# Performance work log

Measured on AMD Instinct MI355X. Metric: run time of the kernel, lower is better.

## Reference

```python
import jax, jax.numpy as jnp
import numpy as np
from math import sqrt

B, N, M, HID, NH = 16, 512, 1024, 512, 8
HS = HID // NH  # 64


def layer_norm(x, g, b, eps=1e-5):
    mu = jnp.mean(x, axis=-1, keepdims=True)
    var = jnp.var(x, axis=-1, keepdims=True)
    return (x - mu) * jax.lax.rsqrt(var + eps) * g + b


def apply_moverz(x, s, c):
    # x: [B, L, NH, HS]; s, c: [B, L, 1, HS//2]
    x0, x1 = x[..., 0::2], x[..., 1::2]
    return jnp.concatenate([x0 * c - x1 * s, x1 * c + x0 * s], axis=-1)


def attention(q, k, v, mask):
    # q: [B,Nq,NH,HS], k/v: [B,Nk,NH,HS], mask broadcastable to [B,NH,Nq,Nk]
    attn = jnp.einsum('bnhd,bmhd->bhnm', q, k) / sqrt(HS)
    attn = jnp.where(mask, -jnp.inf, attn)
    attn = jax.nn.softmax(attn, axis=-1)
    x = jnp.einsum('bhnm,bmhd->bnhd', attn, v)
    return x.reshape(x.shape[0], x.shape[1], HID)


def setup_inputs() -> dict:
    key = jax.random.key(0)
    ks = jax.random.split(key, 24)
    inp = {}
    inp['tgt'] = jax.random.normal(ks[0], (B, N, HID), dtype=jnp.float32)
    inp['mem'] = jax.random.normal(ks[1], (B, M, HID), dtype=jnp.float32)
    th_p = jax.random.uniform(ks[2], (B, N, 1, HS // 2), dtype=jnp.float32) * (2 * np.pi)
    th_k = jax.random.uniform(ks[3], (B, M, 1, HS // 2), dtype=jnp.float32) * (2 * np.pi)
    inp['pep_mass_sin'] = jnp.sin(th_p)
    inp['pep_mass_cos'] = jnp.cos(th_p)
    inp['peaks_moverz_sin'] = jnp.sin(th_k)
    inp['peaks_moverz_cos'] = jnp.cos(th_k)
    # causal self-attn mask (True = masked)
    inp['tgt_mask'] = jnp.triu(jnp.ones((N, N), dtype=bool), k=1)[None, None]
    # pad last 64 memory positions
    pad = jnp.arange(M) >= (M - 64)
    inp['mem_key_padding_mask'] = jnp.broadcast_to(pad[None, None, None, :], (B, 1, 1, M))
    s = 0.02
    w = lambda i, shape: jax.random.normal(ks[i], shape, dtype=jnp.float32) * s
    # MaskedMultiHeadAttn params
    inp['mmha_w'] = w(4, (3 * HID, HID)); inp['mmha_b'] = jnp.zeros((3 * HID,), jnp.float32)
    inp['mmha_ow'] = w(5, (HID, HID)); inp['mmha_ob'] = jnp.zeros((HID,), jnp.float32)
    inp['mmha_g'] = jnp.ones((HID,), jnp.float32); inp['mmha_beta'] = jnp.zeros((HID,), jnp.float32)
    # MultiHeadAttn (cross) params
    inp['mha_qw'] = w(6, (HID, HID)); inp['mha_qb'] = jnp.zeros((HID,), jnp.float32)
    inp['mha_kvw'] = w(7, (2 * HID, HID)); inp['mha_kvb'] = jnp.zeros((2 * HID,), jnp.float32)
    inp['mha_ow'] = w(8, (HID, HID)); inp['mha_ob'] = jnp.zeros((HID,), jnp.float32)
    inp['mha_g'] = jnp.ones((HID,), jnp.float32); inp['mha_beta'] = jnp.zeros((HID,), jnp.float32)
    # FFN params (no bias)
    inp['ffn_w1'] = w(9, (4 * HID, HID))
    inp['ffn_w2'] = w(10, (HID, 4 * HID))
    inp['ffn_g'] = jnp.ones((HID,), jnp.float32); inp['ffn_beta'] = jnp.zeros((HID,), jnp.float32)
    return inp


def reference(tgt, mem, pep_mass_sin, pep_mass_cos, peaks_moverz_sin, peaks_moverz_cos,
              tgt_mask, mem_key_padding_mask,
              mmha_w, mmha_b, mmha_ow, mmha_ob, mmha_g, mmha_beta,
              mha_qw, mha_qb, mha_kvw, mha_kvb, mha_ow, mha_ob, mha_g, mha_beta,
              ffn_w1, ffn_w2, ffn_g, ffn_beta):
    # --- masked self-attention ---
    qkv = (tgt @ mmha_w.T + mmha_b).reshape(B, N, NH, 3 * HS)
    q, k, v = jnp.split(qkv, 3, axis=-1)
    x = attention(q, k, v, tgt_mask)
    tgt = layer_norm(x @ mmha_ow.T + mmha_ob + tgt, mmha_g, mmha_beta)
    # --- cross-attention with moverz distance bias ---
    q = (tgt @ mha_qw.T + mha_qb).reshape(B, N, NH, HS)
    q = apply_moverz(q, pep_mass_sin, pep_mass_cos)
    kv = (mem @ mha_kvw.T + mha_kvb).reshape(B, M, NH, 2 * HS)
    k, v = jnp.split(kv, 2, axis=-1)
    k = apply_moverz(k, peaks_moverz_sin, peaks_moverz_cos)
    x = attention(q, k, v, mem_key_padding_mask)
    tgt = layer_norm(x @ mha_ow.T + mha_ob + tgt, mha_g, mha_beta)
    # --- FFN ---
    h = jax.nn.relu(tgt @ ffn_w1.T) @ ffn_w2.T
    tgt = layer_norm(tgt + h, ffn_g, ffn_beta)
    return tgt
```

## Files before the change

### kernel.cpp

```cpp
#include <hip/hip_runtime.h>
#include <hip/hip_bf16.h>

#define BB 16
#define NN 512
#define MM 1024
#define HIDD 512
#define NHH 8

typedef unsigned short ushort_t;
typedef __attribute__((ext_vector_type(8))) short short8;
typedef __attribute__((ext_vector_type(8))) _Float16 half8;
typedef __attribute__((ext_vector_type(4))) _Float16 half4;
typedef __attribute__((ext_vector_type(4))) float f32x4;

__device__ __forceinline__ ushort_t f2bf(float x) {
    unsigned u = __float_as_uint(x);
    u += 0x7fff + ((u >> 16) & 1);
    return (ushort_t)(u >> 16);
}

#define GLD16(g, l) __builtin_amdgcn_global_load_lds(                      \
    (const __attribute__((address_space(1))) void*)(g),                    \
    (__attribute__((address_space(3))) void*)(l), 16, 0, 0)

__device__ __forceinline__ void xcd_swizzle(int& colb, int& rowb) {
    int id = blockIdx.x + blockIdx.y * gridDim.x;
    int C = gridDim.x;
    int xcd = id & 7;
    int slot = id >> 3;
    int rows_per = gridDim.y >> 3;
    colb = slot % C;
    rowb = xcd * rows_per + slot / C;
}

__global__ __launch_bounds__(256)
void gemm_bf(const ushort_t* __restrict__ A, const ushort_t* __restrict__ W,
             const float* __restrict__ bias, float* __restrict__ C,
             ushort_t* __restrict__ Cb, _Float16* __restrict__ Ch,
             int K, int Cout, int relu) {
    __shared__ __align__(16) ushort_t smem[2][8192];
    const int tid = threadIdx.x;
    const int lane = tid & 63;
    const int wid = tid >> 6;
    const int wm = wid >> 1, wn = wid & 1;
    int colb, rowb;
    xcd_swizzle(colb, rowb);
    const long row0 = (long)rowb * 128;
    const long col0 = (long)colb * 128;

    const int sr = lane >> 2;
    const int skq = lane & 3;
    const ushort_t* Ag = A + (row0 + wid * 32 + sr) * (long)K + skq * 8;
    const ushort_t* Wg = W + (col0 + wid * 32 + sr) * (long)K + skq * 8;
    const int sa0 = (wid * 32) * 32, sa1 = (wid * 32 + 16) * 32;

    f32x4 acc[4][4] = {};
    const int lr = lane & 15;
    const int kg = lane >> 4;

    GLD16(Ag, &smem[0][sa0]);
    GLD16(Ag + 16 * (long)K, &smem[0][sa1]);
    GLD16(Wg, &smem[0][4096 + sa0]);
    GLD16(Wg + 16 * (long)K, &smem[0][4096 + sa1]);

    int pb = 0;
    for (int k0 = 0; k0 < K; k0 += 32, pb ^= 1) {
        __syncthreads();
        int kn = k0 + 32;
        if (kn < K) {
            GLD16(Ag + kn, &smem[pb ^ 1][sa0]);
            GLD16(Ag + 16 * (long)K + kn, &smem[pb ^ 1][sa1]);
            GLD16(Wg + kn, &smem[pb ^ 1][4096 + sa0]);
            GLD16(Wg + 16 * (long)K + kn, &smem[pb ^ 1][4096 + sa1]);
        }
        const ushort_t* Ab = smem[pb];
        const ushort_t* Wb = smem[pb] + 4096;
        short8 af[4], bfr[4];
#pragma unroll
        for (int i = 0; i < 4; i++)
            af[i] = *(const short8*)&Ab[(wm * 64 + i * 16 + lr) * 32 + kg * 8];
#pragma unroll
        for (int j = 0; j < 4; j++)
            bfr[j] = *(const short8*)&Wb[(wn * 64 + j * 16 + lr) * 32 + kg * 8];
#pragma unroll
        for (int i = 0; i < 4; i++)
#pragma unroll
            for (int j = 0; j < 4; j++)
                acc[i][j] = __builtin_amdgcn_mfma_f32_16x16x32_bf16(
                    af[i], bfr[j], acc[i][j], 0, 0, 0);
    }

#pragma unroll
    for (int i = 0; i < 4; i++) {
#pragma unroll
        for (int j = 0; j < 4; j++) {
            long row = row0 + wm * 64 + i * 16 + kg * 4;
            long col = col0 + wn * 64 + j * 16 + lr;
            float bv = bias ? bias[col] : 0.f;
#pragma unroll
            for (int r = 0; r < 4; r++) {
                float x = acc[i][j][r] + bv;
                if (relu) x = fmaxf(x, 0.f);
                size_t idx = (row + r) * (size_t)Cout + col;
                if (Ch)      Ch[idx] = (_Float16)x;
                else if (Cb) Cb[idx] = f2bf(x);
                else         C[idx] = x;
            }
        }
    }
}

__global__ __launch_bounds__(256)
void gemm_bf64(const ushort_t* __restrict__ A, const ushort_t* __restrict__ W,
               const float* __restrict__ bias, float* __restrict__ C,
               ushort_t* __restrict__ Cb, _Float16* __restrict__ Ch,
               int K, int Cout, int relu) {
    __shared__ __align__(16) ushort_t smem[2][6144];
    const int tid = threadIdx.x;
    const int lane = tid & 63;
    const int w = tid >> 6;
    int colb, rowb;
    xcd_swizzle(colb, rowb);
    const long row0 = (long)rowb * 128;
    const long col0 = (long)colb * 64;

    const int sr = lane >> 2;
    const int skq = lane & 3;
    const ushort_t* Ag = A + (row0 + w * 32 + sr) * (long)K + skq * 8;
    const ushort_t* Wg = W + (col0 + w * 16 + sr) * (long)K + skq * 8;
    const int sa0 = (w * 32) * 32, sa1 = (w * 32 + 16) * 32;
    const int sw0 = 4096 + (w * 16) * 32;

    f32x4 acc[2][4] = {};
    const int lr = lane & 15;
    const int kg = lane >> 4;

    GLD16(Ag, &smem[0][sa0]);
    GLD16(Ag + 16 * (long)K, &smem[0][sa1]);
    GLD16(Wg, &smem[0][sw0]);

    int pb = 0;
    for (int k0 = 0; k0 < K; k0 += 32, pb ^= 1) {
        __syncthreads();
        int kn = k0 + 32;
        if (kn < K) {
            GLD16(Ag + kn, &smem[pb ^ 1][sa0]);
            GLD16(Ag + 16 * (long)K + kn, &smem[pb ^ 1][sa1]);
            GLD16(Wg + kn, &smem[pb ^ 1][sw0]);
        }
        const ushort_t* Ab = smem[pb];
        const ushort_t* Wb = smem[pb] + 4096;
        short8 af[2], bfr[4];
#pragma unroll
        for (int i = 0; i < 2; i++)
            af[i] = *(const short8*)&Ab[(w * 32 + i * 16 + lr) * 32 + kg * 8];
#pragma unroll
        for (int j = 0; j < 4; j++)
            bfr[j] = *(const short8*)&Wb[(j * 16 + lr) * 32 + kg * 8];
#pragma unroll
        for (int i = 0; i < 2; i++)
#pragma unroll
            for (int j = 0; j < 4; j++)
                acc[i][j] = __builtin_amdgcn_mfma_f32_16x16x32_bf16(
                    af[i], bfr[j], acc[i][j], 0, 0, 0);
    }

#pragma unroll
    for (int i = 0; i < 2; i++) {
#pragma unroll
        for (int j = 0; j < 4; j++) {
            long row = row0 + w * 32 + i * 16 + kg * 4;
            long col = col0 + j * 16 + lr;
            float bv = bias ? bias[col] : 0.f;
#pragma unroll
            for (int r = 0; r < 4; r++) {
                float x = acc[i][j][r] + bv;
                if (relu) x = fmaxf(x, 0.f);
                size_t idx = (row + r) * (size_t)Cout + col;
                if (Ch)      Ch[idx] = (_Float16)x;
                else if (Cb) Cb[idx] = f2bf(x);
                else         C[idx] = x;
            }
        }
    }
}

__global__ __launch_bounds__(256)
void gemm_q_rot(const ushort_t* __restrict__ A, const ushort_t* __restrict__ W,
                const float* __restrict__ bias,
                const float* __restrict__ sn, const float* __restrict__ cs,
                _Float16* __restrict__ Qrot) {
    __shared__ __align__(16) ushort_t smem[2][6144];
    _Float16* Cs = (_Float16*)smem;
    const int K = 512;
    const int tid = threadIdx.x;
    const int lane = tid & 63;
    const int w = tid >> 6;
    int colb, rowb;
    xcd_swizzle(colb, rowb);
    const long row0 = (long)rowb * 128;
    const int h = colb;
    const long col0 = (long)h * 64;

    const int sr = lane >> 2;
    const int skq = lane & 3;
    const ushort_t* Ag = A + (row0 + w * 32 + sr) * (long)K + skq * 8;
    const ushort_t* Wg = W + (col0 + w * 16 + sr) * (long)K + skq * 8;
    const int sa0 = (w * 32) * 32, sa1 = (w * 32 + 16) * 32;
    const int sw0 = 4096 + (w * 16) * 32;

    f32x4 acc[2][4] = {};
    const int lr = lane & 15;
    const int kg = lane >> 4;

    GLD16(Ag, &smem[0][sa0]);
    GLD16(Ag + 16 * (long)K, &smem[0][sa1]);
    GLD16(Wg, &smem[0][sw0]);

    int pb = 0;
    for (int k0 = 0; k0 < K; k0 += 32, pb ^= 1) {
        __syncthreads();
        int kn = k0 + 32;
        if (kn < K) {
            GLD16(Ag + kn, &smem[pb ^ 1][sa0]);
            GLD16(Ag + 16 * (long)K + kn, &smem[pb ^ 1][sa1]);
            GLD16(Wg + kn, &smem[pb ^ 1][sw0]);
        }
        const ushort_t* Ab = smem[pb];
        const ushort_t* Wb = smem[pb] + 4096;
        short8 af[2], bfr[4];
#pragma unroll
        for (int i = 0; i < 2; i++)
            af[i] = *(const short8*)&Ab[(w * 32 + i * 16 + lr) * 32 + kg * 8];
#pragma unroll
        for (int j = 0; j < 4; j++)
            bfr[j] = *(const short8*)&Wb[(j * 16 + lr) * 32 + kg * 8];
#pragma unroll
        for (int i = 0; i < 2; i++)
#pragma unroll
            for (int j = 0; j < 4; j++)
                acc[i][j] = __builtin_amdgcn_mfma_f32_16x16x32_bf16(
                    af[i], bfr[j], acc[i][j], 0, 0, 0);
    }

    __syncthreads();
#pragma unroll
    for (int i = 0; i < 2; i++)
#pragma unroll
        for (int j = 0; j < 4; j++) {
            int row = w * 32 + i * 16 + kg * 4;
            int col = j * 16 + lr;
            float bv = bias[col0 + col];
#pragma unroll
            for (int r = 0; r < 4; r++)
                Cs[(row + r) * 76 + col] = (_Float16)(acc[i][j][r] + bv);
        }
    __syncthreads();
    for (int idx = tid; idx < 4096; idx += 256) {
        int rr = idx >> 5, j = idx & 31;
        size_t srow = (size_t)row0 + rr;
        float x0 = (float)Cs[rr * 76 + 2 * j], x1 = (float)Cs[rr * 76 + 2 * j + 1];
        float s = sn[srow * 32 + j], c = cs[srow * 32 + j];
        Qrot[srow * 512 + h * 64 + j]      = (_Float16)(x0 * c - x1 * s);
        Qrot[srow * 512 + h * 64 + 32 + j] = (_Float16)(x1 * c + x0 * s);
    }
}

__global__ __launch_bounds__(256)
void gemm_kv(const ushort_t* __restrict__ A, const ushort_t* __restrict__ W,
             const float* __restrict__ bias,
             const float* __restrict__ sn, const float* __restrict__ cs,
             _Float16* __restrict__ Krot, _Float16* __restrict__ Vth) {
    __shared__ __align__(16) ushort_t smem[2][8192];
    _Float16* Cs = (_Float16*)smem;
    const int K = 512;
    const int tid = threadIdx.x;
    const int lane = tid & 63;
    const int wid = tid >> 6;
    const int wm = wid >> 1, wn = wid & 1;
    int colb, rowb;
    xcd_swizzle(colb, rowb);
    const long row0 = (long)rowb * 128;
    const int h = colb;
    const long col0 = (long)h * 128;

    const int sr = lane >> 2;
    const int skq = lane & 3;
    const ushort_t* Ag = A + (row0 + wid * 32 + sr) * (long)K + skq * 8;
    const ushort_t* Wg = W + (col0 + wid * 32 + sr) * (long)K + skq * 8;
    const int sa0 = (wid * 32) * 32, sa1 = (wid * 32 + 16) * 32;

    f32x4 acc[4][4] = {};
    const int lr = lane & 15;
    const int kg = lane >> 4;

    GLD16(Ag, &smem[0][sa0]);
    GLD16(Ag + 16 * (long)K, &smem[0][sa1]);
    GLD16(Wg, &smem[0][4096 + sa0]);
    GLD16(Wg + 16 * (long)K, &smem[0][4096 + sa1]);

    int pb = 0;
    for (int k0 = 0; k0 < K; k0 += 32, pb ^= 1) {
        __syncthreads();
        int kn = k0 + 32;
        if (kn < K) {
            GLD16(Ag + kn, &smem[pb ^ 1][sa0]);
            GLD16(Ag + 16 * (long)K + kn, &smem[pb ^ 1][sa1]);
            GLD16(Wg + kn, &smem[pb ^ 1][4096 + sa0]);
            GLD16(Wg + 16 * (long)K + kn, &smem[pb ^ 1][4096 + sa1]);
        }
        const ushort_t* Ab = smem[pb];
        const ushort_t* Wb = smem[pb] + 4096;
        short8 af[4], bfr[4];
#pragma unroll
        for (int i = 0; i < 4; i++)
            af[i] = *(const short8*)&Ab[(wm * 64 + i * 16 + lr) * 32 + kg * 8];
#pragma unroll
        for (int j = 0; j < 4; j++)
            bfr[j] = *(const short8*)&Wb[(wn * 64 + j * 16 + lr) * 32 + kg * 8];
#pragma unroll
        for (int i = 0; i < 4; i++)
#pragma unroll
            for (int j = 0; j < 4; j++)
                acc[i][j] = __builtin_amdgcn_mfma_f32_16x16x32_bf16(
                    af[i], bfr[j], acc[i][j], 0, 0, 0);
    }

    const int b_ = (int)(row0 >> 10);
    const int m0_ = (int)(row0 & 1023);
#pragma unroll
    for (int half = 0; half < 2; half++) {
        __syncthreads();
        if (wn == half) {
#pragma unroll
            for (int i = 0; i < 4; i++)
#pragma unroll
                for (int j = 0; j < 4; j++) {
                    int row = wm * 64 + i * 16 + kg * 4;
                    int col = j * 16 + lr;
                    float bv = bias[col0 + half * 64 + col];
#pragma unroll
                    for (int r = 0; r < 4; r++)
                        Cs[(row + r) * 76 + col] = (_Float16)(acc[i][j][r] + bv);
                }
        }
        __syncthreads();
        if (half == 0) {
            for (int idx = tid; idx < 4096; idx += 256) {
                int rr = idx >> 5, j = idx & 31;
                size_t srow = (size_t)row0 + rr;
                float x0 = (float)Cs[rr * 76 + 2 * j], x1 = (float)Cs[rr * 76 + 2 * j + 1];
                float s = sn[srow * 32 + j], c = cs[srow * 32 + j];
                Krot[srow * 512 + h * 64 + j]      = (_Float16)(x0 * c - x1 * s);
                Krot[srow * 512 + h * 64 + 32 + j] = (_Float16)(x1 * c + x0 * s);
            }
        } else {
            for (int idx = tid; idx < 1024; idx += 256) {
                int d = idx >> 4, c = idx & 15;
                half8 v;
#pragma unroll
                for (int k = 0; k < 8; k++) v[k] = Cs[(c * 8 + k) * 76 + d];
                *(half8*)(Vth + (((size_t)(b_ * NHH + h)) * 64 + d) * MM
                          + m0_ + c * 8) = v;
            }
        }
    }
}

__global__ __launch_bounds__(256)
void cvt_all(const float* __restrict__ tgt, const float* __restrict__ mem,
             const float* __restrict__ w0, const float* __restrict__ w1,
             const float* __restrict__ w2, const float* __restrict__ w3,
             const float* __restrict__ w4, const float* __restrict__ w5,
             const float* __restrict__ w6,
             ushort_t* __restrict__ Abf, ushort_t* __restrict__ membf,
             ushort_t* __restrict__ Wbf) {
    int blk = blockIdx.x;
    const float* src;
    ushort_t* dst;
    size_t off;
    if (blk < 4096)       { src = tgt; dst = Abf;   off = (size_t)blk * 1024; }
    else if (blk < 12288) { src = mem; dst = membf; off = (size_t)(blk - 4096) * 1024; }
    else {
        int wb = blk - 12288;
        dst = Wbf + (size_t)wb * 1024;
        if (wb < 768)       { src = w0; off = (size_t)wb * 1024; }
        else if (wb < 1024) { src = w1; off = (size_t)(wb - 768) * 1024; }
        else if (wb < 1280) { src = w2; off = (size_t)(wb - 1024) * 1024; }
        else if (wb < 1792) { src = w3; off = (size_t)(wb - 1280) * 1024; }
        else if (wb < 2048) { src = w4; off = (size_t)(wb - 1792) * 1024; }
        else if (wb < 3072) { src = w5; off = (size_t)(wb - 2048) * 1024; }
        else                { src = w6; off = (size_t)(wb - 3072) * 1024; }
        float4 v = *(const float4*)(src + off + threadIdx.x * 4);
        ushort4 o;
        o.x = f2bf(v.x); o.y = f2bf(v.y); o.z = f2bf(v.z); o.w = f2bf(v.w);
        *(ushort4*)(dst + threadIdx.x * 4) = o;
        return;
    }
    float4 v = *(const float4*)(src + off + threadIdx.x * 4);
    ushort4 o;
    o.x = f2bf(v.x); o.y = f2bf(v.y); o.z = f2bf(v.z); o.w = f2bf(v.w);
    *(ushort4*)(dst + off + threadIdx.x * 4) = o;
}

__global__ __launch_bounds__(256)
void prep_vt(const _Float16* __restrict__ src, int L, int stride,
             int hmul, int hadd, _Float16* __restrict__ Vt) {
    const int b = blockIdx.z, h = blockIdx.y, m0 = blockIdx.x * 64;
    const int tid = threadIdx.x;
    __shared__ _Float16 vt[64][72];
    for (int idx = tid; idx < 512; idx += 256) {
        int m = idx >> 3, c = idx & 7;
        half8 v = *(const half8*)(src + ((size_t)(b * L + m0 + m)) * stride
                                  + h * hmul + hadd + c * 8);
#pragma unroll
        for (int k = 0; k < 8; k++) vt[c * 8 + k][m] = v[k];
    }
    __syncthreads();
    for (int idx = tid; idx < 512; idx += 256) {
        int d = idx >> 3, c = idx & 7;
        *(half8*)(Vt + (((size_t)(b * NHH + h)) * 64 + d) * L + m0 + c * 8)
            = *(const half8*)&vt[d][c * 8];
    }
}

__global__ __launch_bounds__(512, 4)
void attn8(const _Float16* __restrict__ Q, int qstride, int qmul, int qadd,
           const _Float16* __restrict__ K, int kstride, int kmul, int kadd,
           const _Float16* __restrict__ Vt, int LV, int Lrows,
           ushort_t* __restrict__ out, int kvlen, int causal) {
    const int g = blockIdx.x;
    const int bh = (g & 7) * 16 + ((g >> 3) & 15);
    const int qb = g >> 7;
    const int b = bh >> 3, h = bh & 7;
    const int n0 = qb * 128;
    const int tid = threadIdx.x, lane = tid & 63, w = tid >> 6;
    const int quad = lane >> 4, l16 = lane & 15;
    const int qw = n0 + w * 16;

    __shared__ _Float16 Ks[2][64 * 64];
    __shared__ _Float16 Vs[2][64 * 64];
    __shared__ _Float16 Ps[8][16 * 64];
    _Float16* Pw = Ps[w];

    half8 bq[2];
#pragma unroll
    for (int c = 0; c < 2; c++)
        bq[c] = *(const half8*)(Q + ((size_t)(b * NN + qw + l16)) * qstride
                                + h * qmul + qadd + c * 32 + quad * 8);

    f32x4 acc[4] = {};
    float mrun = -3e38f, lrun = 0.f;

    const int srow = tid >> 3;
    const int scol = tid & 7;
    const int ssw = (scol ^ (srow & 7)) * 8;

    const int limit = causal ? (n0 + 128) : kvlen;
    const int nt = limit >> 6;

    const size_t kbase = ((size_t)(b * Lrows)) * kstride + h * kmul + kadd;
    const size_t vbase = (((size_t)(b * NHH + h)) * 64 + srow) * (size_t)LV;

    half8 kr = *(const half8*)(K + kbase + (size_t)srow * kstride + scol * 8);
    half8 vr = *(const half8*)(Vt + vbase + scol * 8);
    *(half8*)&Ks[0][srow * 64 + ssw] = kr;
    *(half8*)&Vs[0][srow * 64 + ssw] = vr;
    if (nt > 1) {
        kr = *(const half8*)(K + kbase + (size_t)(64 + srow) * kstride + scol * 8);
        vr = *(const half8*)(Vt + vbase + 64 + scol * 8);
    }

    const float SC = 0.125f * 1.44269504f;
    const int fsw = l16 & 7;
    int pb = 0;
    for (int t = 0; t < nt; t++, pb ^= 1) {
        const int key0 = t * 64;
        __syncthreads();
        if (t + 1 < nt) {
            *(half8*)&Ks[pb ^ 1][srow * 64 + ssw] = kr;
            *(half8*)&Vs[pb ^ 1][srow * 64 + ssw] = vr;
            if (t + 2 < nt) {
                kr = *(const half8*)(K + kbase
                        + (size_t)((t + 2) * 64 + srow) * kstride + scol * 8);
                vr = *(const half8*)(Vt + vbase + (t + 2) * 64 + scol * 8);
            }
        }
        if (causal && key0 > qw + 15) continue;

        const _Float16* Kb = Ks[pb];
        const _Float16* Vb = Vs[pb];
        f32x4 st[4];
        __builtin_amdgcn_s_setprio(1);
#pragma unroll
        for (int kt = 0; kt < 4; kt++) {
            const int rk = kt * 16 + l16;
            half8 ak0 = *(const half8*)&Kb[rk * 64 + ((quad ^ fsw) * 8)];
            half8 ak1 = *(const half8*)&Kb[rk * 64 + (((quad + 4) ^ fsw) * 8)];
            f32x4 z = {};
            z = __builtin_amdgcn_mfma_f32_16x16x32_f16(ak0, bq[0], z, 0, 0, 0);
            z = __builtin_amdgcn_mfma_f32_16x16x32_f16(ak1, bq[1], z, 0, 0, 0);
            st[kt] = z;
        }
        __builtin_amdgcn_s_setprio(0);

        if (causal && key0 + 64 > qw) {
            const int qabs = qw + l16;
#pragma unroll
            for (int kt = 0; kt < 4; kt++)
#pragma unroll
                for (int r = 0; r < 4; r++)
                    if (key0 + kt * 16 + quad * 4 + r > qabs)
                        st[kt][r] = -3e38f;
        }

        float lm = -3e38f;
#pragma unroll
        for (int kt = 0; kt < 4; kt++)
            lm = fmaxf(lm, fmaxf(fmaxf(st[kt][0], st[kt][1]),
                                 fmaxf(st[kt][2], st[kt][3])));
        lm = fmaxf(lm, __shfl_xor(lm, 16));
        lm = fmaxf(lm, __shfl_xor(lm, 32));

        const int keep = __all(lm - mrun <= 64.f);
        float corr = 0.f;
        if (!keep) {
            float mnew = fmaxf(mrun, lm);
            corr = exp2f((mrun - mnew) * SC);
            mrun = mnew;
        }
        const float mb = mrun * SC;
        float ls = 0.f;
#pragma unroll
        for (int kt = 0; kt < 4; kt++) {
            half4 ph;
#pragma unroll
            for (int r = 0; r < 4; r++) {
                float p = exp2f(__builtin_fmaf(st[kt][r], SC, -mb));
                ls += p;
                ph[r] = (_Float16)p;
            }
            int jc = 2 * kt + (quad >> 1);
            *(half4*)&Pw[l16 * 64 + ((jc ^ fsw) * 8) + (quad & 1) * 4] = ph;
        }
        ls += __shfl_xor(ls, 16);
        ls += __shfl_xor(ls, 32);
        if (keep) {
            lrun += ls;
        } else {
            lrun = lrun * corr + ls;
            float cb0 = __shfl(corr, (lane & 48) | (quad * 4 + 0));
            float cb1 = __shfl(corr, (lane & 48) | (quad * 4 + 1));
            float cb2 = __shfl(corr, (lane & 48) | (quad * 4 + 2));
            float cb3 = __shfl(corr, (lane & 48) | (quad * 4 + 3));
#pragma unroll
            for (int dt = 0; dt < 4; dt++) {
                acc[dt][0] *= cb0; acc[dt][1] *= cb1;
                acc[dt][2] *= cb2; acc[dt][3] *= cb3;
            }
        }
        half8 ap[2];
#pragma unroll
        for (int c = 0; c < 2; c++)
            ap[c] = *(const half8*)&Pw[l16 * 64 + (((c * 4 + quad) ^ fsw) * 8)];
        __builtin_amdgcn_s_setprio(1);
#pragma unroll
        for (int dt = 0; dt < 4; dt++) {
            const int rv = dt * 16 + l16;
            half8 bv0 = *(const half8*)&Vb[rv * 64 + ((quad ^ fsw) * 8)];
            half8 bv1 = *(const half8*)&Vb[rv * 64 + (((quad + 4) ^ fsw) * 8)];
            acc[dt] = __builtin_amdgcn_mfma_f32_16x16x32_f16(ap[0], bv0, acc[dt], 0, 0, 0);
            acc[dt] = __builtin_amdgcn_mfma_f32_16x16x32_f16(ap[1], bv1, acc[dt], 0, 0, 0);
        }
        __builtin_amdgcn_s_setprio(0);
    }

    float invq = 1.f / lrun;
    float iv0 = __shfl(invq, (lane & 48) | (quad * 4 + 0));
    float iv1 = __shfl(invq, (lane & 48) | (quad * 4 + 1));
    float iv2 = __shfl(invq, (lane & 48) | (quad * 4 + 2));
    float iv3 = __shfl(invq, (lane & 48) | (quad * 4 + 3));
#pragma unroll
    for (int dt = 0; dt < 4; dt++) {
        size_t base = ((size_t)(b * NN + qw + quad * 4)) * 512
                      + h * 64 + dt * 16 + l16;
        out[base]           = f2bf(acc[dt][0] * iv0);
        out[base + 512]     = f2bf(acc[dt][1] * iv1);
        out[base + 1024]    = f2bf(acc[dt][2] * iv2);
        out[base + 1536]    = f2bf(acc[dt][3] * iv3);
    }
}

__global__ __launch_bounds__(256)
void ln_residual(const float* __restrict__ u, int nsplit,
                 const float* __restrict__ res,
                 const float* __restrict__ g, const float* __restrict__ be,
                 float* __restrict__ out, ushort_t* __restrict__ outbf) {
    const int row = blockIdx.x, t = threadIdx.x;
    const float* rp = res + (size_t)row * HIDD;
    float z0 = rp[t];
    float z1 = rp[t + 256];
    for (int s = 0; s < nsplit; s++) {
        const float* up = u + (size_t)s * 4194304 + (size_t)row * HIDD;
        z0 += up[t];
        z1 += up[t + 256];
    }
    float sm = z0 + z1, s2 = z0 * z0 + z1 * z1;
#pragma unroll
    for (int off = 1; off < 64; off <<= 1) {
        sm += __shfl_xor(sm, off, 64);
        s2 += __shfl_xor(s2, off, 64);
    }
    __shared__ float ps[4], ps2[4];
    int w = t >> 6;
    if ((t & 63) == 0) { ps[w] = sm; ps2[w] = s2; }
    __syncthreads();
    sm = ps[0] + ps[1] + ps[2] + ps[3];
    s2 = ps2[0] + ps2[1] + ps2[2] + ps2[3];
    float mu = sm * (1.f / 512.f);
    float var = s2 * (1.f / 512.f) - mu * mu;
    float rstd = rsqrtf(var + 1e-5f);
    float y0 = (z0 - mu) * rstd * g[t] + be[t];
    float y1 = (z1 - mu) * rstd * g[t + 256] + be[t + 256];
    out[(size_t)row * HIDD + t]       = y0;
    out[(size_t)row * HIDD + t + 256] = y1;
    if (outbf) {
        outbf[(size_t)row * HIDD + t]       = f2bf(y0);
        outbf[(size_t)row * HIDD + t + 256] = f2bf(y1);
    }
}

extern "C" void kernel_launch(void* const* d_in, const int* in_sizes, int n_in,
                              void* d_out, int out_size, void* d_ws, size_t ws_size,
                              hipStream_t stream) {
    const float* tgt      = (const float*)d_in[0];
    const float* mem      = (const float*)d_in[1];
    const float* pep_sin  = (const float*)d_in[2];
    const float* pep_cos  = (const float*)d_in[3];
    const float* pk_sin   = (const float*)d_in[4];
    const float* pk_cos   = (const float*)d_in[5];
    const float* mmha_w   = (const float*)d_in[8];
    const float* mmha_b   = (const float*)d_in[9];
    const float* mmha_ow  = (const float*)d_in[10];
    const float* mmha_ob  = (const float*)d_in[11];
    const float* mmha_g   = (const float*)d_in[12];
    const float* mmha_be  = (const float*)d_in[13];
    const float* mha_qw   = (const float*)d_in[14];
    const float* mha_qb   = (const float*)d_in[15];
    const float* mha_kvw  = (const float*)d_in[16];
    const float* mha_kvb  = (const float*)d_in[17];
    const float* mha_ow   = (const float*)d_in[18];
    const float* mha_ob   = (const float*)d_in[19];
    const float* mha_g    = (const float*)d_in[20];
    const float* mha_be   = (const float*)d_in[21];
    const float* ffn_w1   = (const float*)d_in[22];
    const float* ffn_w2   = (const float*)d_in[23];
    const float* ffn_g    = (const float*)d_in[24];
    const float* ffn_be   = (const float*)d_in[25];

    float* ws = (float*)d_ws;
    float* utmp  = ws;
    float* tgt12 = ws + 4194304;
    _Float16* hp = (_Float16*)(ws + 8388608);
    _Float16* qkvh  = hp;
    _Float16* Qrot  = hp + 12582912;
    _Float16* Vth   = hp + 16777216;
    _Float16* Krot  = hp + 25165824;
    ushort_t* membf = (ushort_t*)(hp + 33554432);
    ushort_t* Abf   = (ushort_t*)(hp + 41943040);
    ushort_t* Wbf   = (ushort_t*)(hp + 46137344);
    ushort_t* w_mmha = Wbf;
    ushort_t* w_mmow = Wbf + 786432;
    ushort_t* w_qw   = Wbf + 1048576;
    ushort_t* w_kvw  = Wbf + 1310720;
    ushort_t* w_mow  = Wbf + 1835008;
    ushort_t* w_f1   = Wbf + 2097152;
    ushort_t* w_f2   = Wbf + 3145728;
    ushort_t* hbf = (ushort_t*)qkvh;
    float* out = (float*)d_out;
    (void)in_sizes; (void)n_in; (void)out_size; (void)ws_size;

    cvt_all<<<16384, 256, 0, stream>>>(tgt, mem, mmha_w, mmha_ow, mha_qw,
                                       mha_kvw, mha_ow, ffn_w1, ffn_w2,
                                       Abf, membf, Wbf);
    gemm_bf<<<dim3(12, 64), 256, 0, stream>>>(Abf, w_mmha, mmha_b, nullptr, nullptr, qkvh, 512, 1536, 0);
    prep_vt<<<dim3(8, NHH, BB), 256, 0, stream>>>(qkvh, NN, 1536, 192, 128, Vth);
    attn8<<<512, 512, 0, stream>>>(qkvh, 1536, 192, 0, qkvh, 1536, 192, 64,
                                   Vth, NN, NN, Abf, 0, 1);
    gemm_bf64<<<dim3(8, 64), 256, 0, stream>>>(Abf, w_mmow, mmha_ob, utmp, nullptr, nullptr, 512, 512, 0);
    ln_residual<<<8192, 256, 0, stream>>>(utmp, 1, tgt, mmha_g, mmha_be, tgt12, Abf);
    gemm_q_rot<<<dim3(8, 64), 256, 0, stream>>>(Abf, w_qw, mha_qb, pep_sin, pep_cos, Qrot);
    gemm_kv<<<dim3(8, 128), 256, 0, stream>>>(membf, w_kvw, mha_kvb, pk_sin, pk_cos, Krot, Vth);
    attn8<<<512, 512, 0, stream>>>(Qrot, 512, 64, 0, Krot, 512, 64, 0,
                                   Vth, MM, MM, Abf, MM - 64, 0);
    gemm_bf64<<<dim3(8, 64), 256, 0, stream>>>(Abf, w_mow, mha_ob, utmp, nullptr, nullptr, 512, 512, 0);
    ln_residual<<<8192, 256, 0, stream>>>(utmp, 1, tgt12, mha_g, mha_be, tgt12, Abf);
    gemm_bf<<<dim3(16, 64), 256, 0, stream>>>(Abf, w_f1, nullptr, nullptr, hbf, nullptr, 512, 2048, 1);
    gemm_bf64<<<dim3(8, 64), 256, 0, stream>>>(hbf, w_f2, nullptr, utmp, nullptr, nullptr, 2048, 512, 0);
    ln_residual<<<8192, 256, 0, stream>>>(utmp, 1, tgt12, ffn_g, ffn_be, out, nullptr);
}
```

Measured before the change: 399.5 us.

## Process 128 keys per attention iteration and split-K the FFN down-projection

The attention kernel now stages 128 keys per loop iteration, using two 64-key halves for the scores, softmax and PV MMAs. This halves the number of barriers and loop iterations. Padding and causal masking are now applied explicitly, and the second half is skipped when it is fully causally masked. The FFN second GEMM is split along K into two slices that write separate partial buffers, and the final layernorm sums them. This doubles the grid for better CU fill. The cost is doubled K/V LDS buffers, which may lower attention occupancy, plus extra partial-sum traffic.

```diff
diff --git a/kernel.cpp b/kernel.cpp
--- a/kernel.cpp
+++ b/kernel.cpp
@@ -183,6 +183,74 @@
             }
         }
     }
+}
+
+__global__ __launch_bounds__(256)
+void gemm_bf64_sk(const ushort_t* __restrict__ A, const ushort_t* __restrict__ W,
+                  int lda, int Kslice, float* __restrict__ C0,
+                  float* __restrict__ C1, int Cout) {
+    __shared__ __align__(16) ushort_t smem[2][6144];
+    const int tid = threadIdx.x;
+    const int lane = tid & 63;
+    const int w = tid >> 6;
+    int colb, rowb;
+    xcd_swizzle(colb, rowb);
+    const long row0 = (long)rowb * 128;
+    const long col0 = (long)colb * 64;
+    const long koff = (long)blockIdx.z * Kslice;
+    float* __restrict__ C = blockIdx.z ? C1 : C0;
+
+    const int sr = lane >> 2;
+    const int skq = lane & 3;
+    const ushort_t* Ag = A + (row0 + w * 32 + sr) * (long)lda + koff + skq * 8;
+    const ushort_t* Wg = W + (col0 + w * 16 + sr) * (long)lda + koff + skq * 8;
+    const int sa0 = (w * 32) * 32, sa1 = (w * 32 + 16) * 32;
+    const int sw0 = 4096 + (w * 16) * 32;
+
+    f32x4 acc[2][4] = {};
+    const int lr = lane & 15;
+    const int kg = lane >> 4;
+
+    GLD16(Ag, &smem[0][sa0]);
+    GLD16(Ag + 16 * (long)lda, &smem[0][sa1]);
+    GLD16(Wg, &smem[0][sw0]);
+
+    int pb = 0;
+    for (int k0 = 0; k0 < Kslice; k0 += 32, pb ^= 1) {
+        __syncthreads();
+        int kn = k0 + 32;
+        if (kn < Kslice) {
+            GLD16(Ag + kn, &smem[pb ^ 1][sa0]);
+            GLD16(Ag + 16 * (long)lda + kn, &smem[pb ^ 1][sa1]);
+            GLD16(Wg + kn, &smem[pb ^ 1][sw0]);
+        }
+        const ushort_t* Ab = smem[pb];
+        const ushort_t* Wb = smem[pb] + 4096;
+        short8 af[2], bfr[4];
+#pragma unroll
+        for (int i = 0; i < 2; i++)
+            af[i] = *(const short8*)&Ab[(w * 32 + i * 16 + lr) * 32 + kg * 8];
+#pragma unroll
+        for (int j = 0; j < 4; j++)
+            bfr[j] = *(const short8*)&Wb[(j * 16 + lr) * 32 + kg * 8];
+#pragma unroll
+        for (int i = 0; i < 2; i++)
+#pragma unroll
+            for (int j = 0; j < 4; j++)
+                acc[i][j] = __builtin_amdgcn_mfma_f32_16x16x32_bf16(
+                    af[i], bfr[j], acc[i][j], 0, 0, 0);
+    }
+
+#pragma unroll
+    for (int i = 0; i < 2; i++)
+#pragma unroll
+        for (int j = 0; j < 4; j++) {
+            long row = row0 + w * 32 + i * 16 + kg * 4;
+            long col = col0 + j * 16 + lr;
+#pragma unroll
+            for (int r = 0; r < 4; r++)
+                C[(row + r) * (size_t)Cout + col] = acc[i][j][r];
+        }
 }
 
 __global__ __launch_bounds__(256)
@@ -425,7 +493,7 @@
 }
 
 __global__ __launch_bounds__(512, 4)
-void attn8(const _Float16* __restrict__ Q, int qstride, int qmul, int qadd,
+void attn9(const _Float16* __restrict__ Q, int qstride, int qmul, int qadd,
            const _Float16* __restrict__ K, int kstride, int kmul, int kadd,
            const _Float16* __restrict__ Vt, int LV, int Lrows,
            ushort_t* __restrict__ out, int kvlen, int causal) {
@@ -438,8 +506,8 @@
     const int quad = lane >> 4, l16 = lane & 15;
     const int qw = n0 + w * 16;
 
-    __shared__ _Float16 Ks[2][64 * 64];
-    __shared__ _Float16 Vs[2][64 * 64];
+    __shared__ _Float16 Ks[2][128 * 64];
+    __shared__ _Float16 Vs[2][64 * 128];
     __shared__ _Float16 Ps[8][16 * 64];
     _Float16* Pw = Ps[w];
 
@@ -454,43 +522,56 @@
 
     const int srow = tid >> 3;
     const int scol = tid & 7;
-    const int ssw = (scol ^ (srow & 7)) * 8;
+    const int ksw = (scol ^ (srow & 7)) * 8;
+    const int vsw = (scol ^ (srow & 7)) * 8;
 
     const int limit = causal ? (n0 + 128) : kvlen;
-    const int nt = limit >> 6;
+    const int nit = (limit + 127) >> 7;
 
     const size_t kbase = ((size_t)(b * Lrows)) * kstride + h * kmul + kadd;
     const size_t vbase = (((size_t)(b * NHH + h)) * 64 + srow) * (size_t)LV;
 
-    half8 kr = *(const half8*)(K + kbase + (size_t)srow * kstride + scol * 8);
-    half8 vr = *(const half8*)(Vt + vbase + scol * 8);
-    *(half8*)&Ks[0][srow * 64 + ssw] = kr;
-    *(half8*)&Vs[0][srow * 64 + ssw] = vr;
-    if (nt > 1) {
-        kr = *(const half8*)(K + kbase + (size_t)(64 + srow) * kstride + scol * 8);
-        vr = *(const half8*)(Vt + vbase + 64 + scol * 8);
+    half8 kr0 = *(const half8*)(K + kbase + (size_t)srow * kstride + scol * 8);
+    half8 kr1 = *(const half8*)(K + kbase + (size_t)(64 + srow) * kstride + scol * 8);
+    half8 vr0 = *(const half8*)(Vt + vbase + scol * 8);
+    half8 vr1 = *(const half8*)(Vt + vbase + 64 + scol * 8);
+    *(half8*)&Ks[0][srow * 64 + ksw] = kr0;
+    *(half8*)&Ks[0][(64 + srow) * 64 + ksw] = kr1;
+    *(half8*)&Vs[0][srow * 128 + vsw] = vr0;
+    *(half8*)&Vs[0][srow * 128 + vsw + 64] = vr1;
+    if (nit > 1) {
+        kr0 = *(const half8*)(K + kbase + (size_t)(128 + srow) * kstride + scol * 8);
+        kr1 = *(const half8*)(K + kbase + (size_t)(192 + srow) * kstride + scol * 8);
+        vr0 = *(const half8*)(Vt + vbase + 128 + scol * 8);
+        vr1 = *(const half8*)(Vt + vbase + 192 + scol * 8);
     }
 
     const float SC = 0.125f * 1.44269504f;
     const int fsw = l16 & 7;
     int pb = 0;
-    for (int t = 0; t < nt; t++, pb ^= 1) {
-        const int key0 = t * 64;
+    for (int it = 0; it < nit; it++, pb ^= 1) {
+        const int key0 = it * 128;
         __syncthreads();
-        if (t + 1 < nt) {
-            *(half8*)&Ks[pb ^ 1][srow * 64 + ssw] = kr;
-            *(half8*)&Vs[pb ^ 1][srow * 64 + ssw] = vr;
-            if (t + 2 < nt) {
-                kr = *(const half8*)(K + kbase
-                        + (size_t)((t + 2) * 64 + srow) * kstride + scol * 8);
-                vr = *(const half8*)(Vt + vbase + (t + 2) * 64 + scol * 8);
+        if (it + 1 < nit) {
+            *(half8*)&Ks[pb ^ 1][srow * 64 + ksw] = kr0;
+            *(half8*)&Ks[pb ^ 1][(64 + srow) * 64 + ksw] = kr1;
+            *(half8*)&Vs[pb ^ 1][srow * 128 + vsw] = vr0;
+            *(half8*)&Vs[pb ^ 1][srow * 128 + vsw + 64] = vr1;
+            if (it + 2 < nit) {
+                const int r0 = (it + 2) * 128;
+                kr0 = *(const half8*)(K + kbase + (size_t)(r0 + srow) * kstride + scol * 8);
+                kr1 = *(const half8*)(K + kbase + (size_t)(r0 + 64 + srow) * kstride + scol * 8);
+                vr0 = *(const half8*)(Vt + vbase + r0 + scol * 8);
+                vr1 = *(const half8*)(Vt + vbase + r0 + 64 + scol * 8);
             }
         }
         if (causal && key0 > qw + 15) continue;
 
         const _Float16* Kb = Ks[pb];
         const _Float16* Vb = Vs[pb];
-        f32x4 st[4];
+        const int do1 = (!causal) || (key0 + 64 <= qw + 15);
+
+        f32x4 st0[4], st1[4];
         __builtin_amdgcn_s_setprio(1);
 #pragma unroll
         for (int kt = 0; kt < 4; kt++) {
@@ -500,25 +581,68 @@
             f32x4 z = {};
             z = __builtin_amdgcn_mfma_f32_16x16x32_f16(ak0, bq[0], z, 0, 0, 0);
             z = __builtin_amdgcn_mfma_f32_16x16x32_f16(ak1, bq[1], z, 0, 0, 0);
-            st[kt] = z;
+            st0[kt] = z;
+        }
+        if (do1) {
+#pragma unroll
+            for (int kt = 0; kt < 4; kt++) {
+                const int rk = 64 + kt * 16 + l16;
+                half8 ak0 = *(const half8*)&Kb[rk * 64 + ((quad ^ fsw) * 8)];
+                half8 ak1 = *(const half8*)&Kb[rk * 64 + (((quad + 4) ^ fsw) * 8)];
+                f32x4 z = {};
+                z = __builtin_amdgcn_mfma_f32_16x16x32_f16(ak0, bq[0], z, 0, 0, 0);
+                z = __builtin_amdgcn_mfma_f32_16x16x32_f16(ak1, bq[1], z, 0, 0, 0);
+                st1[kt] = z;
+            }
         }
         __builtin_amdgcn_s_setprio(0);
 
-        if (causal && key0 + 64 > qw) {
-            const int qabs = qw + l16;
+        const int qabs = qw + l16;
+        if (causal) {
+            if (key0 + 64 > qw) {
+#pragma unroll
+                for (int kt = 0; kt < 4; kt++)
+#pragma unroll
+                    for (int r = 0; r < 4; r++)
+                        if (key0 + kt * 16 + quad * 4 + r > qabs)
+                            st0[kt][r] = -3e38f;
+            }
+            if (do1 && key0 + 128 > qw) {
+#pragma unroll
+                for (int kt = 0; kt < 4; kt++)
+#pragma unroll
+                    for (int r = 0; r < 4; r++)
+                        if (key0 + 64 + kt * 16 + quad * 4 + r > qabs)
+                            st1[kt][r] = -3e38f;
+            }
+        } else if (key0 + 128 > kvlen) {
+            if (key0 + 64 > kvlen) {
+#pragma unroll
+                for (int kt = 0; kt < 4; kt++)
+#pragma unroll
+                    for (int r = 0; r < 4; r++)
+                        if (key0 + kt * 16 + quad * 4 + r >= kvlen)
+                            st0[kt][r] = -3e38f;
+            }
 #pragma unroll
             for (int kt = 0; kt < 4; kt++)
 #pragma unroll
                 for (int r = 0; r < 4; r++)
-                    if (key0 + kt * 16 + quad * 4 + r > qabs)
-                        st[kt][r] = -3e38f;
+                    if (key0 + 64 + kt * 16 + quad * 4 + r >= kvlen)
+                        st1[kt][r] = -3e38f;
         }
 
         float lm = -3e38f;
 #pragma unroll
         for (int kt = 0; kt < 4; kt++)
-            lm = fmaxf(lm, fmaxf(fmaxf(st[kt][0], st[kt][1]),
-                                 fmaxf(st[kt][2], st[kt][3])));
+            lm = fmaxf(lm, fmaxf(fmaxf(st0[kt][0], st0[kt][1]),
+                                 fmaxf(st0[kt][2], st0[kt][3])));
+        if (do1) {
+#pragma unroll
+            for (int kt = 0; kt < 4; kt++)
+                lm = fmaxf(lm, fmaxf(fmaxf(st1[kt][0], st1[kt][1]),
+                                     fmaxf(st1[kt][2], st1[kt][3])));
+        }
         lm = fmaxf(lm, __shfl_xor(lm, 16));
         lm = fmaxf(lm, __shfl_xor(lm, 32));
 
@@ -536,12 +660,34 @@
             half4 ph;
 #pragma unroll
             for (int r = 0; r < 4; r++) {
-                float p = exp2f(__builtin_fmaf(st[kt][r], SC, -mb));
+                float p = exp2f(__builtin_fmaf(st0[kt][r], SC, -mb));
                 ls += p;
                 ph[r] = (_Float16)p;
             }
             int jc = 2 * kt + (quad >> 1);
             *(half4*)&Pw[l16 * 64 + ((jc ^ fsw) * 8) + (quad & 1) * 4] = ph;
+        }
+        half8 ap0[2];
+#pragma unroll
+        for (int c = 0; c < 2; c++)
+            ap0[c] = *(const half8*)&Pw[l16 * 64 + (((c * 4 + quad) ^ fsw) * 8)];
+        half8 ap1[2];
+        if (do1) {
+#pragma unroll
+            for (int kt = 0; kt < 4; kt++) {
+                half4 ph;
+#pragma unroll
+                for (int r = 0; r < 4; r++) {
+                    float p = exp2f(__builtin_fmaf(st1[kt][r], SC, -mb));
+                    ls += p;
+                    ph[r] = (_Float16)p;
+                }
+                int jc = 2 * kt + (quad >> 1);
+                *(half4*)&Pw[l16 * 64 + ((jc ^ fsw) * 8) + (quad & 1) * 4] = ph;
+            }
+#pragma unroll
+            for (int c = 0; c < 2; c++)
+                ap1[c] = *(const half8*)&Pw[l16 * 64 + (((c * 4 + quad) ^ fsw) * 8)];
         }
         ls += __shfl_xor(ls, 16);
         ls += __shfl_xor(ls, 32);
@@ -559,18 +705,24 @@
                 acc[dt][2] *= cb2; acc[dt][3] *= cb3;
             }
         }
-        half8 ap[2];
-#pragma unroll
-        for (int c = 0; c < 2; c++)
-            ap[c] = *(const half8*)&Pw[l16 * 64 + (((c * 4 + quad) ^ fsw) * 8)];
         __builtin_amdgcn_s_setprio(1);
 #pragma unroll
         for (int dt = 0; dt < 4; dt++) {
             const int rv = dt * 16 + l16;
-            half8 bv0 = *(const half8*)&Vb[rv * 64 + ((quad ^ fsw) * 8)];
-            half8 bv1 = *(const half8*)&Vb[rv * 64 + (((quad + 4) ^ fsw) * 8)];
-            acc[dt] = __builtin_amdgcn_mfma_f32_16x16x32_f16(ap[0], bv0, acc[dt], 0, 0, 0);
-            acc[dt] = __builtin_amdgcn_mfma_f32_16x16x32_f16(ap[1], bv1, acc[dt], 0, 0, 0);
+            half8 bv0 = *(const half8*)&Vb[rv * 128 + ((quad ^ fsw) * 8)];
+            half8 bv1 = *(const half8*)&Vb[rv * 128 + (((quad + 4) ^ fsw) * 8)];
+            acc[dt] = __builtin_amdgcn_mfma_f32_16x16x32_f16(ap0[0], bv0, acc[dt], 0, 0, 0);
+            acc[dt] = __builtin_amdgcn_mfma_f32_16x16x32_f16(ap0[1], bv1, acc[dt], 0, 0, 0);
+        }
+        if (do1) {
+#pragma unroll
+            for (int dt = 0; dt < 4; dt++) {
+                const int rv = dt * 16 + l16;
+                half8 bv0 = *(const half8*)&Vb[rv * 128 + 64 + ((quad ^ fsw) * 8)];
+                half8 bv1 = *(const half8*)&Vb[rv * 128 + 64 + (((quad + 4) ^ fsw) * 8)];
+                acc[dt] = __builtin_amdgcn_mfma_f32_16x16x32_f16(ap1[0], bv0, acc[dt], 0, 0, 0);
+                acc[dt] = __builtin_amdgcn_mfma_f32_16x16x32_f16(ap1[1], bv1, acc[dt], 0, 0, 0);
+            }
         }
         __builtin_amdgcn_s_setprio(0);
     }
@@ -592,18 +744,19 @@
 }
 
 __global__ __launch_bounds__(256)
-void ln_residual(const float* __restrict__ u, int nsplit,
+void ln_residual(const float* __restrict__ u, const float* __restrict__ u2,
                  const float* __restrict__ res,
                  const float* __restrict__ g, const float* __restrict__ be,
                  float* __restrict__ out, ushort_t* __restrict__ outbf) {
     const int row = blockIdx.x, t = threadIdx.x;
     const float* rp = res + (size_t)row * HIDD;
-    float z0 = rp[t];
-    float z1 = rp[t + 256];
-    for (int s = 0; s < nsplit; s++) {
-        const float* up = u + (size_t)s * 4194304 + (size_t)row * HIDD;
-        z0 += up[t];
-        z1 += up[t + 256];
+    const float* up = u + (size_t)row * HIDD;
+    float z0 = rp[t] + up[t];
+    float z1 = rp[t + 256] + up[t + 256];
+    if (u2) {
+        const float* up2 = u2 + (size_t)row * HIDD;
+        z0 += up2[t];
+        z1 += up2[t + 256];
     }
     float sm = z0 + z1, s2 = z0 * z0 + z1 * z1;
 #pragma unroll
@@ -677,6 +830,7 @@
     ushort_t* w_f1   = Wbf + 2097152;
     ushort_t* w_f2   = Wbf + 3145728;
     ushort_t* hbf = (ushort_t*)qkvh;
+    float* utmp2 = (float*)Krot;
     float* out = (float*)d_out;
     (void)in_sizes; (void)n_in; (void)out_size; (void)ws_size;
 
@@ -685,17 +839,17 @@
                                        Abf, membf, Wbf);
     gemm_bf<<<dim3(12, 64), 256, 0, stream>>>(Abf, w_mmha, mmha_b, nullptr, nullptr, qkvh, 512, 1536, 0);
     prep_vt<<<dim3(8, NHH, BB), 256, 0, stream>>>(qkvh, NN, 1536, 192, 128, Vth);
-    attn8<<<512, 512, 0, stream>>>(qkvh, 1536, 192, 0, qkvh, 1536, 192, 64,
+    attn9<<<512, 512, 0, stream>>>(qkvh, 1536, 192, 0, qkvh, 1536, 192, 64,
                                    Vth, NN, NN, Abf, 0, 1);
     gemm_bf64<<<dim3(8, 64), 256, 0, stream>>>(Abf, w_mmow, mmha_ob, utmp, nullptr, nullptr, 512, 512, 0);
-    ln_residual<<<8192, 256, 0, stream>>>(utmp, 1, tgt, mmha_g, mmha_be, tgt12, Abf);
+    ln_residual<<<8192, 256, 0, stream>>>(utmp, nullptr, tgt, mmha_g, mmha_be, tgt12, Abf);
     gemm_q_rot<<<dim3(8, 64), 256, 0, stream>>>(Abf, w_qw, mha_qb, pep_sin, pep_cos, Qrot);
     gemm_kv<<<dim3(8, 128), 256, 0, stream>>>(membf, w_kvw, mha_kvb, pk_sin, pk_cos, Krot, Vth);
-    attn8<<<512, 512, 0, stream>>>(Qrot, 512, 64, 0, Krot, 512, 64, 0,
+    attn9<<<512, 512, 0, stream>>>(Qrot, 512, 64, 0, Krot, 512, 64, 0,
                                    Vth, MM, MM, Abf, MM - 64, 0);
     gemm_bf64<<<dim3(8, 64), 256, 0, stream>>>(Abf, w_mow, mha_ob, utmp, nullptr, nullptr, 512, 512, 0);
-    ln_residual<<<8192, 256, 0, stream>>>(utmp, 1, tgt12, mha_g, mha_be, tgt12, Abf);
+    ln_residual<<<8192, 256, 0, stream>>>(utmp, nullptr, tgt12, mha_g, mha_be, tgt12, Abf);
     gemm_bf<<<dim3(16, 64), 256, 0, stream>>>(Abf, w_f1, nullptr, nullptr, hbf, nullptr, 512, 2048, 1);
-    gemm_bf64<<<dim3(8, 64), 256, 0, stream>>>(hbf, w_f2, nullptr, utmp, nullptr, nullptr, 2048, 512, 0);
-    ln_residual<<<8192, 256, 0, stream>>>(utmp, 1, tgt12, ffn_g, ffn_be, out, nullptr);
-}
+    gemm_bf64_sk<<<dim3(8, 64, 2), 256, 0, stream>>>(hbf, w_f2, 2048, 1024, utmp, utmp2, 512);
+    ln_residual<<<8192, 256, 0, stream>>>(utmp, utmp2, tgt12, ffn_g, ffn_be, out, nullptr);
+}
```

Result: slower. 425.9 us (+6.6%).

## Split-K the FFN down-projection and defer softmax row-sum reduction in attention

Applied to the files above, without the earlier changes.

Adds a split-K variant of the 64-wide GEMM for the FFN second projection. It writes two partial outputs that the layer-norm kernel sums, which doubles the grid on a K=2048 GEMM that otherwise launches few blocks. The attention kernel becomes attn10. It keeps per-lane partial row sums and reduces them only once at the end, does the max shuffle only when a rescale is needed, packs probabilities with cvt_pkrtz, and swaps query-block order to balance causal work. The cost is extra fp32 partial-output traffic, reuse of the Krot buffer as scratch, and round-toward-zero fp16 conversion.

```diff
diff --git a/kernel.cpp b/kernel.cpp
--- a/kernel.cpp
+++ b/kernel.cpp
@@ -11,6 +11,7 @@
 typedef __attribute__((ext_vector_type(8))) short short8;
 typedef __attribute__((ext_vector_type(8))) _Float16 half8;
 typedef __attribute__((ext_vector_type(4))) _Float16 half4;
+typedef __attribute__((ext_vector_type(2))) __fp16 fp16x2;
 typedef __attribute__((ext_vector_type(4))) float f32x4;
 
 __device__ __forceinline__ ushort_t f2bf(float x) {
@@ -183,6 +184,74 @@
             }
         }
     }
+}
+
+__global__ __launch_bounds__(256)
+void gemm_bf64_sk(const ushort_t* __restrict__ A, const ushort_t* __restrict__ W,
+                  int lda, int Kslice, float* __restrict__ C0,
+                  float* __restrict__ C1, int Cout) {
+    __shared__ __align__(16) ushort_t smem[2][6144];
+    const int tid = threadIdx.x;
+    const int lane = tid & 63;
+    const int w = tid >> 6;
+    int colb, rowb;
+    xcd_swizzle(colb, rowb);
+    const long row0 = (long)rowb * 128;
+    const long col0 = (long)colb * 64;
+    const long koff = (long)blockIdx.z * Kslice;
+    float* __restrict__ C = blockIdx.z ? C1 : C0;
+
+    const int sr = lane >> 2;
+    const int skq = lane & 3;
+    const ushort_t* Ag = A + (row0 + w * 32 + sr) * (long)lda + koff + skq * 8;
+    const ushort_t* Wg = W + (col0 + w * 16 + sr) * (long)lda + koff + skq * 8;
+    const int sa0 = (w * 32) * 32, sa1 = (w * 32 + 16) * 32;
+    const int sw0 = 4096 + (w * 16) * 32;
+
+    f32x4 acc[2][4] = {};
+    const int lr = lane & 15;
+    const int kg = lane >> 4;
+
+    GLD16(Ag, &smem[0][sa0]);
+    GLD16(Ag + 16 * (long)lda, &smem[0][sa1]);
+    GLD16(Wg, &smem[0][sw0]);
+
+    int pb = 0;
+    for (int k0 = 0; k0 < Kslice; k0 += 32, pb ^= 1) {
+        __syncthreads();
+        int kn = k0 + 32;
+        if (kn < Kslice) {
+            GLD16(Ag + kn, &smem[pb ^ 1][sa0]);
+            GLD16(Ag + 16 * (long)lda + kn, &smem[pb ^ 1][sa1]);
+            GLD16(Wg + kn, &smem[pb ^ 1][sw0]);
+        }
+        const ushort_t* Ab = smem[pb];
+        const ushort_t* Wb = smem[pb] + 4096;
+        short8 af[2], bfr[4];
+#pragma unroll
+        for (int i = 0; i < 2; i++)
+            af[i] = *(const short8*)&Ab[(w * 32 + i * 16 + lr) * 32 + kg * 8];
+#pragma unroll
+        for (int j = 0; j < 4; j++)
+            bfr[j] = *(const short8*)&Wb[(j * 16 + lr) * 32 + kg * 8];
+#pragma unroll
+        for (int i = 0; i < 2; i++)
+#pragma unroll
+            for (int j = 0; j < 4; j++)
+                acc[i][j] = __builtin_amdgcn_mfma_f32_16x16x32_bf16(
+                    af[i], bfr[j], acc[i][j], 0, 0, 0);
+    }
+
+#pragma unroll
+    for (int i = 0; i < 2; i++)
+#pragma unroll
+        for (int j = 0; j < 4; j++) {
+            long row = row0 + w * 32 + i * 16 + kg * 4;
+            long col = col0 + j * 16 + lr;
+#pragma unroll
+            for (int r = 0; r < 4; r++)
+                C[(row + r) * (size_t)Cout + col] = acc[i][j][r];
+        }
 }
 
 __global__ __launch_bounds__(256)
@@ -425,13 +494,14 @@
 }
 
 __global__ __launch_bounds__(512, 4)
-void attn8(const _Float16* __restrict__ Q, int qstride, int qmul, int qadd,
-           const _Float16* __restrict__ K, int kstride, int kmul, int kadd,
-           const _Float16* __restrict__ Vt, int LV, int Lrows,
-           ushort_t* __restrict__ out, int kvlen, int causal) {
+void attn10(const _Float16* __restrict__ Q, int qstride, int qmul, int qadd,
+            const _Float16* __restrict__ K, int kstride, int kmul, int kadd,
+            const _Float16* __restrict__ Vt, int LV, int Lrows,
+            ushort_t* __restrict__ out, int kvlen, int causal) {
     const int g = blockIdx.x;
     const int bh = (g & 7) * 16 + ((g >> 3) & 15);
-    const int qb = g >> 7;
+    int qb = g >> 7;
+    qb ^= (qb & 2) >> 1;
     const int b = bh >> 3, h = bh & 7;
     const int n0 = qb * 128;
     const int tid = threadIdx.x, lane = tid & 63, w = tid >> 6;
@@ -514,41 +584,20 @@
                         st[kt][r] = -3e38f;
         }
 
-        float lm = -3e38f;
+        float plm = -3e38f;
 #pragma unroll
         for (int kt = 0; kt < 4; kt++)
-            lm = fmaxf(lm, fmaxf(fmaxf(st[kt][0], st[kt][1]),
-                                 fmaxf(st[kt][2], st[kt][3])));
-        lm = fmaxf(lm, __shfl_xor(lm, 16));
-        lm = fmaxf(lm, __shfl_xor(lm, 32));
-
-        const int keep = __all(lm - mrun <= 64.f);
-        float corr = 0.f;
+            plm = fmaxf(plm, fmaxf(fmaxf(st[kt][0], st[kt][1]),
+                                   fmaxf(st[kt][2], st[kt][3])));
+
+        const int keep = __all(plm - mrun <= 64.f);
         if (!keep) {
+            float lm = fmaxf(plm, __shfl_xor(plm, 16));
+            lm = fmaxf(lm, __shfl_xor(lm, 32));
             float mnew = fmaxf(mrun, lm);
-            corr = exp2f((mrun - mnew) * SC);
+            float corr = exp2f((mrun - mnew) * SC);
             mrun = mnew;
-        }
-        const float mb = mrun * SC;
-        float ls = 0.f;
-#pragma unroll
-        for (int kt = 0; kt < 4; kt++) {
-            half4 ph;
-#pragma unroll
-            for (int r = 0; r < 4; r++) {
-                float p = exp2f(__builtin_fmaf(st[kt][r], SC, -mb));
-                ls += p;
-                ph[r] = (_Float16)p;
-            }
-            int jc = 2 * kt + (quad >> 1);
-            *(half4*)&Pw[l16 * 64 + ((jc ^ fsw) * 8) + (quad & 1) * 4] = ph;
-        }
-        ls += __shfl_xor(ls, 16);
-        ls += __shfl_xor(ls, 32);
-        if (keep) {
-            lrun += ls;
-        } else {
-            lrun = lrun * corr + ls;
+            lrun *= corr;
             float cb0 = __shfl(corr, (lane & 48) | (quad * 4 + 0));
             float cb1 = __shfl(corr, (lane & 48) | (quad * 4 + 1));
             float cb2 = __shfl(corr, (lane & 48) | (quad * 4 + 2));
@@ -558,6 +607,22 @@
                 acc[dt][0] *= cb0; acc[dt][1] *= cb1;
                 acc[dt][2] *= cb2; acc[dt][3] *= cb3;
             }
+        }
+        const float mb = mrun * SC;
+#pragma unroll
+        for (int kt = 0; kt < 4; kt++) {
+            float p0 = exp2f(__builtin_fmaf(st[kt][0], SC, -mb));
+            float p1 = exp2f(__builtin_fmaf(st[kt][1], SC, -mb));
+            float p2 = exp2f(__builtin_fmaf(st[kt][2], SC, -mb));
+            float p3 = exp2f(__builtin_fmaf(st[kt][3], SC, -mb));
+            lrun += (p0 + p1) + (p2 + p3);
+            fp16x2 lo = __builtin_amdgcn_cvt_pkrtz(p0, p1);
+            fp16x2 hi = __builtin_amdgcn_cvt_pkrtz(p2, p3);
+            union { unsigned u[2]; half4 h; } pk;
+            pk.u[0] = __builtin_bit_cast(unsigned, lo);
+            pk.u[1] = __builtin_bit_cast(unsigned, hi);
+            int jc = 2 * kt + (quad >> 1);
+            *(half4*)&Pw[l16 * 64 + ((jc ^ fsw) * 8) + (quad & 1) * 4] = pk.h;
         }
         half8 ap[2];
 #pragma unroll
@@ -575,6 +640,8 @@
         __builtin_amdgcn_s_setprio(0);
     }
 
+    lrun += __shfl_xor(lrun, 16);
+    lrun += __shfl_xor(lrun, 32);
     float invq = 1.f / lrun;
     float iv0 = __shfl(invq, (lane & 48) | (quad * 4 + 0));
     float iv1 = __shfl(invq, (lane & 48) | (quad * 4 + 1));
@@ -592,18 +659,19 @@
 }
 
 __global__ __launch_bounds__(256)
-void ln_residual(const float* __restrict__ u, int nsplit,
+void ln_residual(const float* __restrict__ u, const float* __restrict__ u2,
                  const float* __restrict__ res,
                  const float* __restrict__ g, const float* __restrict__ be,
                  float* __restrict__ out, ushort_t* __restrict__ outbf) {
     const int row = blockIdx.x, t = threadIdx.x;
     const float* rp = res + (size_t)row * HIDD;
-    float z0 = rp[t];
-    float z1 = rp[t + 256];
-    for (int s = 0; s < nsplit; s++) {
-        const float* up = u + (size_t)s * 4194304 + (size_t)row * HIDD;
-        z0 += up[t];
-        z1 += up[t + 256];
+    const float* up = u + (size_t)row * HIDD;
+    float z0 = rp[t] + up[t];
+    float z1 = rp[t + 256] + up[t + 256];
+    if (u2) {
+        const float* up2 = u2 + (size_t)row * HIDD;
+        z0 += up2[t];
+        z1 += up2[t + 256];
     }
     float sm = z0 + z1, s2 = z0 * z0 + z1 * z1;
 #pragma unroll
@@ -677,6 +745,7 @@
     ushort_t* w_f1   = Wbf + 2097152;
     ushort_t* w_f2   = Wbf + 3145728;
     ushort_t* hbf = (ushort_t*)qkvh;
+    float* utmp2 = (float*)Krot;
     float* out = (float*)d_out;
     (void)in_sizes; (void)n_in; (void)out_size; (void)ws_size;
 
@@ -685,17 +754,17 @@
                                        Abf, membf, Wbf);
     gemm_bf<<<dim3(12, 64), 256, 0, stream>>>(Abf, w_mmha, mmha_b, nullptr, nullptr, qkvh, 512, 1536, 0);
     prep_vt<<<dim3(8, NHH, BB), 256, 0, stream>>>(qkvh, NN, 1536, 192, 128, Vth);
-    attn8<<<512, 512, 0, stream>>>(qkvh, 1536, 192, 0, qkvh, 1536, 192, 64,
-                                   Vth, NN, NN, Abf, 0, 1);
+    attn10<<<512, 512, 0, stream>>>(qkvh, 1536, 192, 0, qkvh, 1536, 192, 64,
+                                    Vth, NN, NN, Abf, 0, 1);
     gemm_bf64<<<dim3(8, 64), 256, 0, stream>>>(Abf, w_mmow, mmha_ob, utmp, nullptr, nullptr, 512, 512, 0);
-    ln_residual<<<8192, 256, 0, stream>>>(utmp, 1, tgt, mmha_g, mmha_be, tgt12, Abf);
+    ln_residual<<<8192, 256, 0, stream>>>(utmp, nullptr, tgt, mmha_g, mmha_be, tgt12, Abf);
     gemm_q_rot<<<dim3(8, 64), 256, 0, stream>>>(Abf, w_qw, mha_qb, pep_sin, pep_cos, Qrot);
     gemm_kv<<<dim3(8, 128), 256, 0, stream>>>(membf, w_kvw, mha_kvb, pk_sin, pk_cos, Krot, Vth);
-    attn8<<<512, 512, 0, stream>>>(Qrot, 512, 64, 0, Krot, 512, 64, 0,
-                                   Vth, MM, MM, Abf, MM - 64, 0);
+    attn10<<<512, 512, 0, stream>>>(Qrot, 512, 64, 0, Krot, 512, 64, 0,
+                                    Vth, MM, MM, Abf, MM - 64, 0);
     gemm_bf64<<<dim3(8, 64), 256, 0, stream>>>(Abf, w_mow, mha_ob, utmp, nullptr, nullptr, 512, 512, 0);
-    ln_residual<<<8192, 256, 0, stream>>>(utmp, 1, tgt12, mha_g, mha_be, tgt12, Abf);
+    ln_residual<<<8192, 256, 0, stream>>>(utmp, nullptr, tgt12, mha_g, mha_be, tgt12, Abf);
     gemm_bf<<<dim3(16, 64), 256, 0, stream>>>(Abf, w_f1, nullptr, nullptr, hbf, nullptr, 512, 2048, 1);
-    gemm_bf64<<<dim3(8, 64), 256, 0, stream>>>(hbf, w_f2, nullptr, utmp, nullptr, nullptr, 2048, 512, 0);
-    ln_residual<<<8192, 256, 0, stream>>>(utmp, 1, tgt12, ffn_g, ffn_be, out, nullptr);
-}
+    gemm_bf64_sk<<<dim3(8, 64, 2), 256, 0, stream>>>(hbf, w_f2, 2048, 1024, utmp, utmp2, 512);
+    ln_residual<<<8192, 256, 0, stream>>>(utmp, utmp2, tgt12, ffn_g, ffn_be, out, nullptr);
+}
```

Measured after the change: 397.6 us. Within noise of the previous version (-0.5%).
